# Performance work log

Hardware: AMD Instinct MI355X
Metric: run time of the kernel (lower is better)

The kernel has to match this reference:

```python
import jax, jax.numpy as jnp
import numpy as np
from jax.ops import segment_sum

N_NODES = 1_000_000
N_EDGES = 10_000_000


def gcn_conv(x, W, b, src, dst, n_nodes):
    """PyG GCNConv: add self-loops, sym-normalize, linear, scatter-sum, bias."""
    h = x @ W  # [N, out]
    loop = jnp.arange(n_nodes, dtype=src.dtype)
    s = jnp.concatenate([src, loop])  # sources incl. self-loops
    d = jnp.concatenate([dst, loop])  # targets incl. self-loops
    deg = segment_sum(jnp.ones(s.shape[0], dtype=h.dtype), d, num_segments=n_nodes)
    dinv = jnp.where(deg > 0, jax.lax.rsqrt(deg), 0.0)  # deg^-1/2, 0 for isolated
    norm = dinv[s] * dinv[d]  # [E+N]
    msg = h[s] * norm[:, None]  # gather + scale
    out = segment_sum(msg, d, num_segments=n_nodes)  # scatter-add at targets
    return out + b


def setup_inputs() -> dict:
    key = jax.random.key(0)
    k1, k2, k3, k4, k5 = jax.random.split(key, 5)
    x = jax.random.normal(k1, (N_NODES, 3), dtype=jnp.float32)
    edge_index = jax.random.randint(k2, (2, N_EDGES), 0, N_NODES, dtype=jnp.int64)
    # Glorot-ish init for the two GCNConv layers (3->8, 8->2) with bias
    W1 = jax.random.normal(k3, (3, 8), dtype=jnp.float32) * (1.0 / np.sqrt(3.0))
    b1 = jnp.zeros((8,), dtype=jnp.float32)
    W2 = jax.random.normal(k4, (8, 2), dtype=jnp.float32) * (1.0 / np.sqrt(8.0))
    b2 = jnp.zeros((2,), dtype=jnp.float32)
    return {"x": x, "edge_index": edge_index, "W1": W1, "b1": b1, "W2": W2, "b2": b2}


def reference(x, edge_index, W1, b1, W2, b2):
    src, dst = edge_index[0], edge_index[1]
    n = x.shape[0]
    h = gcn_conv(x, W1, b1, src, dst, n)
    h = jax.nn.relu(h)
    return gcn_conv(h, W2, b2, src, dst, n)
```

## Files before the change

### kernel.cpp

```cpp
#include <hip/hip_runtime.h>


#define BSH 12
#define BKT 4096
#define NBKT_MAX 256
#define TILE 4096

__global__ void k_hist(const int* __restrict__ dst, int* __restrict__ bcnt,
                       int e, int nbkt) {
    __shared__ int h[NBKT_MAX];
    int t = threadIdx.x;
    h[t] = 0;
    __syncthreads();
    int stride = gridDim.x * blockDim.x;
    for (int i = blockIdx.x * blockDim.x + t; i < e; i += stride)
        atomicAdd(&h[dst[i] >> BSH], 1);
    __syncthreads();
    if (t < nbkt && h[t]) atomicAdd(&bcnt[t], h[t]);
}

__global__ void k_scan(const int* __restrict__ bcnt, int* __restrict__ bofs,
                       int* __restrict__ bcur, int nbkt) {
    __shared__ int sh[256];
    int t = threadIdx.x;
    int v = (t < nbkt) ? bcnt[t] : 0;
    sh[t] = v;
    __syncthreads();
    for (int off = 1; off < 256; off <<= 1) {
        int w = (t >= off) ? sh[t - off] : 0;
        __syncthreads();
        sh[t] += w;
        __syncthreads();
    }
    if (t < nbkt) {
        int ex = sh[t] - v;
        bofs[t] = ex;
        bcur[t] = ex;
    }
}

__global__ void k_msplit(const int* __restrict__ src, const int* __restrict__ dst,
                         int* __restrict__ bcur, unsigned* __restrict__ esort,
                         int e, int nbkt) {
    __shared__ unsigned stage[TILE];
    __shared__ unsigned char bid[TILE];
    __shared__ int h[NBKT_MAX];
    __shared__ int lscan[NBKT_MAX];
    __shared__ int baseadj[NBKT_MAX];
    int t = threadIdx.x;
    int base = blockIdx.x * TILE;
    int cnt = min(TILE, e - base);
    h[t] = 0;
    __syncthreads();

    unsigned val[16];
    int bk[16], rnk[16];
#pragma unroll
    for (int k = 0; k < 16; ++k) {
        int i = base + k * 256 + t;
        bk[k] = -1;
        if (i < e) {
            int d = dst[i], s = src[i];
            bk[k] = d >> BSH;
            val[k] = ((unsigned)(d & (BKT - 1)) << 20) | (unsigned)s;
            rnk[k] = atomicAdd(&h[bk[k]], 1);
        }
    }
    __syncthreads();
    int c = h[t];
    __syncthreads();
    lscan[t] = c;
    __syncthreads();
    for (int off = 1; off < 256; off <<= 1) {
        int w = (t >= off) ? lscan[t - off] : 0;
        __syncthreads();
        lscan[t] += w;
        __syncthreads();
    }
    int ex = lscan[t] - c;
    __syncthreads();
    lscan[t] = ex;
    if (c > 0) baseadj[t] = atomicAdd(&bcur[t], c) - ex;
    __syncthreads();

#pragma unroll
    for (int k = 0; k < 16; ++k) {
        if (bk[k] >= 0) {
            int idx = lscan[bk[k]] + rnk[k];
            stage[idx] = val[k];
            bid[idx] = (unsigned char)bk[k];
        }
    }
    __syncthreads();
#pragma unroll
    for (int k = 0; k < 16; ++k) {
        int j = k * 256 + t;
        if (j < cnt) esort[baseadj[bid[j]] + j] = stage[j];
    }
}

__global__ void k_deg_xd(const unsigned* __restrict__ esort, const int* __restrict__ bofs,
                         const int* __restrict__ bcnt, const float* __restrict__ x,
                         float4* __restrict__ xd, int n) {
    __shared__ int deg[BKT];
    int b = blockIdx.x, t = threadIdx.x;
#pragma unroll
    for (int k = 0; k < BKT / 256; ++k) deg[k * 256 + t] = 0;
    __syncthreads();
    int beg = bofs[b], end = beg + bcnt[b];
    for (int p = beg + t; p < end; p += 256)
        atomicAdd(&deg[esort[p] >> 20], 1);
    __syncthreads();
#pragma unroll
    for (int k = 0; k < BKT / 256; ++k) {
        int dl = k * 256 + t;
        int node = b * BKT + dl;
        if (node < n) {
            float di = rsqrtf((float)deg[dl] + 1.0f);
            float x0 = x[3 * node], x1 = x[3 * node + 1], x2 = x[3 * node + 2];
            xd[node] = make_float4(x0 * di, x1 * di, x2 * di, di);
        }
    }
}

__global__ void k_l1(const unsigned* __restrict__ esort, const int* __restrict__ bofs,
                     const int* __restrict__ bcnt, const float4* __restrict__ xd,
                     const float* __restrict__ W1, const float* __restrict__ b1,
                     const float* __restrict__ W2, float2* __restrict__ g2, int n) {
    __shared__ float acc[BKT * 3];
    int b = blockIdx.x, t = threadIdx.x;
#pragma unroll
    for (int k = 0; k < BKT * 3 / 256; ++k) acc[k * 256 + t] = 0.0f;
    __syncthreads();
    int beg = bofs[b], end = beg + bcnt[b];
    for (int p = beg + t; p < end; p += 256) {
        unsigned v = esort[p];
        float4 s = xd[v & 0xFFFFFu];
        int dl = v >> 20;
        atomicAdd(&acc[dl * 3 + 0], s.x);
        atomicAdd(&acc[dl * 3 + 1], s.y);
        atomicAdd(&acc[dl * 3 + 2], s.z);
    }
    __syncthreads();
#pragma unroll
    for (int k = 0; k < BKT / 256; ++k) {
        int dl = k * 256 + t;
        int node = b * BKT + dl;
        if (node >= n) continue;
        float4 sd = xd[node];
        float di = sd.w;
        float a0 = (acc[dl * 3 + 0] + sd.x) * di;
        float a1 = (acc[dl * 3 + 1] + sd.y) * di;
        float a2 = (acc[dl * 3 + 2] + sd.z) * di;
        float h0 = 0.0f, h1 = 0.0f;
#pragma unroll
        for (int j = 0; j < 8; ++j) {
            float r = fmaxf(a0 * W1[j] + a1 * W1[8 + j] + a2 * W1[16 + j] + b1[j], 0.0f);
            h0 += r * W2[2 * j + 0];
            h1 += r * W2[2 * j + 1];
        }
        g2[node] = make_float2(h0 * di, h1 * di);
    }
}

__global__ void k_l2(const unsigned* __restrict__ esort, const int* __restrict__ bofs,
                     const int* __restrict__ bcnt, const float4* __restrict__ xd,
                     const float2* __restrict__ g2, const float* __restrict__ b2,
                     float2* __restrict__ out, int n) {
    __shared__ float acc[BKT * 2];
    int b = blockIdx.x, t = threadIdx.x;
#pragma unroll
    for (int k = 0; k < BKT * 2 / 256; ++k) acc[k * 256 + t] = 0.0f;
    __syncthreads();
    int beg = bofs[b], end = beg + bcnt[b];
    for (int p = beg + t; p < end; p += 256) {
        unsigned v = esort[p];
        float2 s = g2[v & 0xFFFFFu];
        int dl = v >> 20;
        atomicAdd(&acc[dl * 2 + 0], s.x);
        atomicAdd(&acc[dl * 2 + 1], s.y);
    }
    __syncthreads();
#pragma unroll
    for (int k = 0; k < BKT / 256; ++k) {
        int dl = k * 256 + t;
        int node = b * BKT + dl;
        if (node >= n) continue;
        float2 sv = g2[node];
        float di = xd[node].w;
        out[node] = make_float2((acc[dl * 2 + 0] + sv.x) * di + b2[0],
                                (acc[dl * 2 + 1] + sv.y) * di + b2[1]);
    }
}

extern "C" void kernel_launch(void* const* d_in, const int* in_sizes, int n_in,
                              void* d_out, int out_size, void* d_ws, size_t ws_size,
                              hipStream_t stream) {
    const float* x  = (const float*)d_in[0];
    const int*   ei = (const int*)d_in[1];
    const float* W1 = (const float*)d_in[2];
    const float* b1 = (const float*)d_in[3];
    const float* W2 = (const float*)d_in[4];
    const float* b2 = (const float*)d_in[5];
    float2* out = (float2*)d_out;

    const int n = in_sizes[0] / 3;
    const int e = in_sizes[1] / 2;
    const int* src = ei;
    const int* dst = ei + e;
    const int nbkt = (n + BKT - 1) >> BSH;

    char* w = (char*)d_ws;
    float4*   xd    = (float4*)w;    w += (size_t)n * sizeof(float4);
    float2*   g2    = (float2*)w;    w += (size_t)n * sizeof(float2);
    unsigned* esort = (unsigned*)w;  w += (size_t)e * sizeof(unsigned);
    int*      bcnt  = (int*)w;       w += (size_t)NBKT_MAX * sizeof(int);
    int*      bofs  = (int*)w;       w += (size_t)NBKT_MAX * sizeof(int);
    int*      bcur  = (int*)w;

    const int B = 256;
    const int nb_ms = (e + TILE - 1) / TILE;

    hipMemsetAsync(bcnt, 0, (size_t)NBKT_MAX * sizeof(int), stream);
    k_hist  <<<512, B, 0, stream>>>(dst, bcnt, e, nbkt);
    k_scan  <<<1, B, 0, stream>>>(bcnt, bofs, bcur, nbkt);
    k_msplit<<<nb_ms, B, 0, stream>>>(src, dst, bcur, esort, e, nbkt);
    k_deg_xd<<<nbkt, B, 0, stream>>>(esort, bofs, bcnt, x, xd, n);
    k_l1    <<<nbkt, B, 0, stream>>>(esort, bofs, bcnt, xd, W1, b1, W2, g2, n);
    k_l2    <<<nbkt, B, 0, stream>>>(esort, bofs, bcnt, xd, g2, b2, out, n);
}
```

Baseline: 443.8 us.

## Split aggregation buckets into four sub-blocks and store layer-2 features as bf16

```diff
diff --git a/kernel.cpp b/kernel.cpp
--- a/kernel.cpp
+++ b/kernel.cpp
@@ -3,8 +3,14 @@
 
 #define BSH 12
 #define BKT 4096
+#define SUBSZ 1024
 #define NBKT_MAX 256
 #define TILE 4096
+
+__device__ inline unsigned bf16r(float f) {
+    unsigned u = __float_as_uint(f);
+    return (u + 0x7FFFu + ((u >> 16) & 1u)) & 0xFFFF0000u;
+}
 
 __global__ void k_hist(const int* __restrict__ dst, int* __restrict__ bcnt,
                        int e, int nbkt) {
@@ -102,19 +108,23 @@
 __global__ void k_deg_xd(const unsigned* __restrict__ esort, const int* __restrict__ bofs,
                          const int* __restrict__ bcnt, const float* __restrict__ x,
                          float4* __restrict__ xd, int n) {
-    __shared__ int deg[BKT];
-    int b = blockIdx.x, t = threadIdx.x;
-#pragma unroll
-    for (int k = 0; k < BKT / 256; ++k) deg[k * 256 + t] = 0;
+    __shared__ int deg[SUBSZ];
+    int b = blockIdx.x >> 2, sub = blockIdx.x & 3;
+    int t = threadIdx.x;
+#pragma unroll
+    for (int k = 0; k < SUBSZ / 256; ++k) deg[k * 256 + t] = 0;
     __syncthreads();
     int beg = bofs[b], end = beg + bcnt[b];
-    for (int p = beg + t; p < end; p += 256)
-        atomicAdd(&deg[esort[p] >> 20], 1);
-    __syncthreads();
-#pragma unroll
-    for (int k = 0; k < BKT / 256; ++k) {
+    for (int p = beg + t; p < end; p += 256) {
+        int dl = esort[p] >> 20;
+        if ((dl >> 10) == sub) atomicAdd(&deg[dl & (SUBSZ - 1)], 1);
+    }
+    __syncthreads();
+    int nbase = (b << BSH) + (sub << 10);
+#pragma unroll
+    for (int k = 0; k < SUBSZ / 256; ++k) {
         int dl = k * 256 + t;
-        int node = b * BKT + dl;
+        int node = nbase + dl;
         if (node < n) {
             float di = rsqrtf((float)deg[dl] + 1.0f);
             float x0 = x[3 * node], x1 = x[3 * node + 1], x2 = x[3 * node + 2];
@@ -126,26 +136,31 @@
 __global__ void k_l1(const unsigned* __restrict__ esort, const int* __restrict__ bofs,
                      const int* __restrict__ bcnt, const float4* __restrict__ xd,
                      const float* __restrict__ W1, const float* __restrict__ b1,
-                     const float* __restrict__ W2, float2* __restrict__ g2, int n) {
-    __shared__ float acc[BKT * 3];
-    int b = blockIdx.x, t = threadIdx.x;
-#pragma unroll
-    for (int k = 0; k < BKT * 3 / 256; ++k) acc[k * 256 + t] = 0.0f;
+                     const float* __restrict__ W2, unsigned* __restrict__ g2, int n) {
+    __shared__ float acc[SUBSZ * 3];
+    int b = blockIdx.x >> 2, sub = blockIdx.x & 3;
+    int t = threadIdx.x;
+#pragma unroll
+    for (int k = 0; k < SUBSZ * 3 / 256; ++k) acc[k * 256 + t] = 0.0f;
     __syncthreads();
     int beg = bofs[b], end = beg + bcnt[b];
     for (int p = beg + t; p < end; p += 256) {
         unsigned v = esort[p];
-        float4 s = xd[v & 0xFFFFFu];
         int dl = v >> 20;
-        atomicAdd(&acc[dl * 3 + 0], s.x);
-        atomicAdd(&acc[dl * 3 + 1], s.y);
-        atomicAdd(&acc[dl * 3 + 2], s.z);
-    }
-    __syncthreads();
-#pragma unroll
-    for (int k = 0; k < BKT / 256; ++k) {
+        if ((dl >> 10) == sub) {
+            float4 s = xd[v & 0xFFFFFu];
+            int q = dl & (SUBSZ - 1);
+            atomicAdd(&acc[q * 3 + 0], s.x);
+            atomicAdd(&acc[q * 3 + 1], s.y);
+            atomicAdd(&acc[q * 3 + 2], s.z);
+        }
+    }
+    __syncthreads();
+    int nbase = (b << BSH) + (sub << 10);
+#pragma unroll
+    for (int k = 0; k < SUBSZ / 256; ++k) {
         int dl = k * 256 + t;
-        int node = b * BKT + dl;
+        int node = nbase + dl;
         if (node >= n) continue;
         float4 sd = xd[node];
         float di = sd.w;
@@ -159,37 +174,44 @@
             h0 += r * W2[2 * j + 0];
             h1 += r * W2[2 * j + 1];
         }
-        g2[node] = make_float2(h0 * di, h1 * di);
+        g2[node] = (bf16r(h0 * di) >> 16) | bf16r(h1 * di);
     }
 }
 
 __global__ void k_l2(const unsigned* __restrict__ esort, const int* __restrict__ bofs,
                      const int* __restrict__ bcnt, const float4* __restrict__ xd,
-                     const float2* __restrict__ g2, const float* __restrict__ b2,
+                     const unsigned* __restrict__ g2, const float* __restrict__ b2,
                      float2* __restrict__ out, int n) {
-    __shared__ float acc[BKT * 2];
-    int b = blockIdx.x, t = threadIdx.x;
-#pragma unroll
-    for (int k = 0; k < BKT * 2 / 256; ++k) acc[k * 256 + t] = 0.0f;
+    __shared__ float acc[SUBSZ * 2];
+    int b = blockIdx.x >> 2, sub = blockIdx.x & 3;
+    int t = threadIdx.x;
+#pragma unroll
+    for (int k = 0; k < SUBSZ * 2 / 256; ++k) acc[k * 256 + t] = 0.0f;
     __syncthreads();
     int beg = bofs[b], end = beg + bcnt[b];
     for (int p = beg + t; p < end; p += 256) {
         unsigned v = esort[p];
-        float2 s = g2[v & 0xFFFFFu];
         int dl = v >> 20;
-        atomicAdd(&acc[dl * 2 + 0], s.x);
-        atomicAdd(&acc[dl * 2 + 1], s.y);
-    }
-    __syncthreads();
-#pragma unroll
-    for (int k = 0; k < BKT / 256; ++k) {
+        if ((dl >> 10) == sub) {
+            unsigned gg = g2[v & 0xFFFFFu];
+            int q = dl & (SUBSZ - 1);
+            atomicAdd(&acc[q * 2 + 0], __uint_as_float(gg << 16));
+            atomicAdd(&acc[q * 2 + 1], __uint_as_float(gg & 0xFFFF0000u));
+        }
+    }
+    __syncthreads();
+    int nbase = (b << BSH) + (sub << 10);
+#pragma unroll
+    for (int k = 0; k < SUBSZ / 256; ++k) {
         int dl = k * 256 + t;
-        int node = b * BKT + dl;
+        int node = nbase + dl;
         if (node >= n) continue;
-        float2 sv = g2[node];
+        unsigned gg = g2[node];
+        float s0 = __uint_as_float(gg << 16);
+        float s1 = __uint_as_float(gg & 0xFFFF0000u);
         float di = xd[node].w;
-        out[node] = make_float2((acc[dl * 2 + 0] + sv.x) * di + b2[0],
-                                (acc[dl * 2 + 1] + sv.y) * di + b2[1]);
+        out[node] = make_float2((acc[dl * 2 + 0] + s0) * di + b2[0],
+                                (acc[dl * 2 + 1] + s1) * di + b2[1]);
     }
 }
 
@@ -212,7 +234,7 @@
 
     char* w = (char*)d_ws;
     float4*   xd    = (float4*)w;    w += (size_t)n * sizeof(float4);
-    float2*   g2    = (float2*)w;    w += (size_t)n * sizeof(float2);
+    unsigned* g2    = (unsigned*)w;  w += (size_t)n * sizeof(unsigned);
     unsigned* esort = (unsigned*)w;  w += (size_t)e * sizeof(unsigned);
     int*      bcnt  = (int*)w;       w += (size_t)NBKT_MAX * sizeof(int);
     int*      bofs  = (int*)w;       w += (size_t)NBKT_MAX * sizeof(int);
@@ -220,12 +242,13 @@
 
     const int B = 256;
     const int nb_ms = (e + TILE - 1) / TILE;
+    const int nb_agg = nbkt * 4;
 
     hipMemsetAsync(bcnt, 0, (size_t)NBKT_MAX * sizeof(int), stream);
     k_hist  <<<512, B, 0, stream>>>(dst, bcnt, e, nbkt);
     k_scan  <<<1, B, 0, stream>>>(bcnt, bofs, bcur, nbkt);
     k_msplit<<<nb_ms, B, 0, stream>>>(src, dst, bcur, esort, e, nbkt);
-    k_deg_xd<<<nbkt, B, 0, stream>>>(esort, bofs, bcnt, x, xd, n);
-    k_l1    <<<nbkt, B, 0, stream>>>(esort, bofs, bcnt, xd, W1, b1, W2, g2, n);
-    k_l2    <<<nbkt, B, 0, stream>>>(esort, bofs, bcnt, xd, g2, b2, out, n);
-}
+    k_deg_xd<<<nb_agg, B, 0, stream>>>(esort, bofs, bcnt, x, xd, n);
+    k_l1    <<<nb_agg, B, 0, stream>>>(esort, bofs, bcnt, xd, W1, b1, W2, g2, n);
+    k_l2    <<<nb_agg, B, 0, stream>>>(esort, bofs, bcnt, xd, g2, b2, out, n);
+}
```

After: 466.5 us. +5.1%, slower.
